# Optimization experiments

Measured on AMD Instinct MI355X. Metric: run time of the kernel, lower is better.

## Reference

```python
import jax, jax.numpy as jnp
import numpy as np

B, T, C, H = 2, 4096, 512, 8
D = C // H          # head_size = 64
FF = 4 * C          # 2048
EPS = 1e-5


def _layernorm(x, g, b):
    mu = jnp.mean(x, axis=-1, keepdims=True)
    var = jnp.mean(jnp.square(x - mu), axis=-1, keepdims=True)
    return (x - mu) * jax.lax.rsqrt(var + EPS) * g + b


def setup_inputs() -> dict:
    key = jax.random.key(0)
    ks = jax.random.split(key, 10)
    s = 0.02
    return {
        "x":  jax.random.normal(ks[0], (B, T, C), dtype=jnp.float32),
        # per-head K/Q/V linears (bias=False) packed as [C, C] = concat over heads
        "Wq": jax.random.normal(ks[1], (C, C), dtype=jnp.float32) * s,
        "Wk": jax.random.normal(ks[2], (C, C), dtype=jnp.float32) * s,
        "Wv": jax.random.normal(ks[3], (C, C), dtype=jnp.float32) * s,
        "Wo": jax.random.normal(ks[4], (C, C), dtype=jnp.float32) * s,
        "bo": jnp.zeros((C,), dtype=jnp.float32),
        "W1": jax.random.normal(ks[5], (C, FF), dtype=jnp.float32) * s,
        "b1": jnp.zeros((FF,), dtype=jnp.float32),
        "W2": jax.random.normal(ks[6], (FF, C), dtype=jnp.float32) * s,
        "b2": jnp.zeros((C,), dtype=jnp.float32),
        "g1": jnp.ones((C,), dtype=jnp.float32),
        "be1": jnp.zeros((C,), dtype=jnp.float32),
        "g2": jnp.ones((C,), dtype=jnp.float32),
        "be2": jnp.zeros((C,), dtype=jnp.float32),
    }


def reference(x, Wq, Wk, Wv, Wo, bo, W1, b1, W2, b2, g1, be1, g2, be2):
    # --- self-attention on ln1(x), residual add ---
    h = _layernorm(x, g1, be1)                              # [B,T,C]
    q = (h @ Wq).reshape(B, T, H, D)
    k = (h @ Wk).reshape(B, T, H, D)
    v = (h @ Wv).reshape(B, T, H, D)
    # NOTE: original scales by C**-0.5 (n_embd), NOT head_size**-0.5
    scores = jnp.einsum("bthd,bshd->bhts", q, k) * (C ** -0.5)  # [B,H,T,T]
    causal = jnp.tril(jnp.ones((T, T), dtype=bool))
    scores = jnp.where(causal, scores, -jnp.inf)
    wei = jax.nn.softmax(scores, axis=-1)                   # dropout = identity (eval)
    attn = jnp.einsum("bhts,bshd->bthd", wei, v).reshape(B, T, C)
    x = x + (attn @ Wo + bo)                                # proj dropout = identity
    # --- feed-forward on ln2(x), residual add ---
    h2 = _layernorm(x, g2, be2)
    ff = jax.nn.relu(h2 @ W1 + b1) @ W2 + b2                # dropout = identity
    return x + ff
```

## Files before the change

kernel.cpp:

```cpp
#include <hip/hip_runtime.h>

typedef __attribute__((ext_vector_type(8))) __bf16 bf16x8;
typedef __attribute__((ext_vector_type(4))) float f32x4;
typedef __attribute__((ext_vector_type(4))) unsigned int u32x4;
typedef __attribute__((ext_vector_type(4))) unsigned short u16x4;
typedef __attribute__((ext_vector_type(8))) unsigned short u16x8;
typedef unsigned short u16;

static __device__ __forceinline__ u16 f2b(float f) {
    unsigned u = __builtin_bit_cast(unsigned, f);
    u = (u + 0x7FFFu + ((u >> 16) & 1u)) >> 16;
    return (u16)u;
}
static __device__ __forceinline__ float b2f(u16 u) {
    return __builtin_bit_cast(float, ((unsigned)u) << 16);
}

static __device__ __forceinline__ void gload16(const u16* g, u16* l) {
    __builtin_amdgcn_global_load_lds(
        (const __attribute__((address_space(1))) unsigned int*)g,
        (__attribute__((address_space(3))) unsigned int*)l, 16, 0, 0);
}

__global__ __launch_bounds__(256) void prep_w(
    const float* __restrict__ Wq, const float* __restrict__ Wk,
    const float* __restrict__ Wv, const float* __restrict__ Wo,
    const float* __restrict__ W1, const float* __restrict__ W2,
    u16* __restrict__ WqkvT, u16* __restrict__ WoT,
    u16* __restrict__ W1T, u16* __restrict__ W2T)
{
    const int z = blockIdx.z;
    const float* src; u16* dst; int K, N;
    if (z == 0)      { src = Wq; dst = WqkvT;             K = 512;  N = 512;  }
    else if (z == 1) { src = Wk; dst = WqkvT + 512*512;   K = 512;  N = 512;  }
    else if (z == 2) { src = Wv; dst = WqkvT + 1024*512;  K = 512;  N = 512;  }
    else if (z == 3) { src = Wo; dst = WoT;               K = 512;  N = 512;  }
    else if (z == 4) { src = W1; dst = W1T;               K = 512;  N = 2048; }
    else             { src = W2; dst = W2T;               K = 2048; N = 512;  }
    const int nt = blockIdx.x * 32, kt = blockIdx.y * 32;
    if (nt >= N || kt >= K) return;
    __shared__ float tile[32][33];
    const int tx = threadIdx.x & 31, ty = threadIdx.x >> 5;
    #pragma unroll
    for (int i = 0; i < 4; ++i)
        tile[ty + i*8][tx] = src[(size_t)(kt + ty + i*8) * N + nt + tx];
    __syncthreads();
    #pragma unroll
    for (int i = 0; i < 4; ++i)
        dst[(size_t)(nt + ty + i*8) * K + kt + tx] = f2b(tile[tx][ty + i*8]);
}

__global__ __launch_bounds__(256) void ln_rows(
    const float* __restrict__ x, const float* __restrict__ g,
    const float* __restrict__ b, u16* __restrict__ out)
{
    const int row = blockIdx.x * 4 + (threadIdx.x >> 6);
    const int lane = threadIdx.x & 63;
    const float* xr = x + (size_t)row * 512;
    f32x4 v0 = *(const f32x4*)(xr + lane * 4);
    f32x4 v1 = *(const f32x4*)(xr + 256 + lane * 4);
    float s = v0[0]+v0[1]+v0[2]+v0[3]+v1[0]+v1[1]+v1[2]+v1[3];
    #pragma unroll
    for (int o = 1; o < 64; o <<= 1) s += __shfl_xor(s, o);
    const float mu = s * (1.0f / 512.0f);
    float s2 = 0.f;
    #pragma unroll
    for (int i = 0; i < 4; ++i) { float d0 = v0[i]-mu, d1 = v1[i]-mu; s2 += d0*d0 + d1*d1; }
    #pragma unroll
    for (int o = 1; o < 64; o <<= 1) s2 += __shfl_xor(s2, o);
    const float inv = rsqrtf(s2 * (1.0f/512.0f) + 1e-5f);
    f32x4 g0 = *(const f32x4*)(g + lane*4), g1 = *(const f32x4*)(g + 256 + lane*4);
    f32x4 b0 = *(const f32x4*)(b + lane*4), b1 = *(const f32x4*)(b + 256 + lane*4);
    u16x4 p0, p1;
    #pragma unroll
    for (int i = 0; i < 4; ++i) {
        p0[i] = f2b((v0[i]-mu)*inv*g0[i] + b0[i]);
        p1[i] = f2b((v1[i]-mu)*inv*g1[i] + b1[i]);
    }
    u16* orow = out + (size_t)row * 512;
    *(u16x4*)(orow + lane*4)       = p0;
    *(u16x4*)(orow + 256 + lane*4) = p1;
}

template<int FLAGS>
__global__ __launch_bounds__(256) void gemm_bt(
    const u16* __restrict__ A, const u16* __restrict__ BT,
    const int N, const int K,
    const float* __restrict__ bias, const float* __restrict__ res,
    void* __restrict__ outv)
{
    __shared__ __attribute__((aligned(16))) u16 As[128*32];
    __shared__ __attribute__((aligned(16))) u16 Bs[128*32];
    const int tid = threadIdx.x, lane = tid & 63, w = tid >> 6;
    const int wr = w >> 1, wc = w & 1;
    const int m0 = blockIdx.y << 7, n0 = blockIdx.x << 7;
    const int g = lane >> 4, c = lane & 15;
    const f32x4 fz = {0.f, 0.f, 0.f, 0.f};

    f32x4 acc[4][4];
    #pragma unroll
    for (int m = 0; m < 4; ++m)
      #pragma unroll
      for (int n = 0; n < 4; ++n) acc[m][n] = fz;

    const int srow = tid >> 2;
    const int scs = (((tid & 3) ^ (srow & 3)) * 8);
    const u16* Ag = A  + (size_t)(m0 + srow)*K + scs;
    const u16* Bg = BT + (size_t)(n0 + srow)*K + scs;
    const size_t rstep = (size_t)64 * K;
    u16* AsW = As + w*512;
    u16* BsW = Bs + w*512;

    const int nkt = K >> 5;
    for (int kt = 0; kt < nkt; ++kt) {
        const int k0 = kt << 5;
        gload16(Ag + k0,         AsW);
        gload16(Ag + rstep + k0, AsW + 2048);
        gload16(Bg + k0,         BsW);
        gload16(Bg + rstep + k0, BsW + 2048);
        __syncthreads();
        bf16x8 af[4], bfr[4];
        #pragma unroll
        for (int m = 0; m < 4; ++m) {
            const int row = wr*64 + m*16 + c;
            af[m] = *(const bf16x8*)(As + row*32 + (((g*16) ^ ((row&3)<<4)) >> 1));
        }
        #pragma unroll
        for (int n = 0; n < 4; ++n) {
            const int row = wc*64 + n*16 + c;
            bfr[n] = *(const bf16x8*)(Bs + row*32 + (((g*16) ^ ((row&3)<<4)) >> 1));
        }
        #pragma unroll
        for (int m = 0; m < 4; ++m)
          #pragma unroll
          for (int n = 0; n < 4; ++n)
            acc[m][n] = __builtin_amdgcn_mfma_f32_16x16x32_bf16(af[m], bfr[n], acc[m][n], 0, 0, 0);
        __syncthreads();
    }

    #pragma unroll
    for (int m = 0; m < 4; ++m) {
        const int row = m0 + wr*64 + m*16 + 4*g;
        #pragma unroll
        for (int n = 0; n < 4; ++n) {
            const int col = n0 + wc*64 + n*16 + c;
            const float bv = (FLAGS & 1) ? bias[col] : 0.0f;
            #pragma unroll
            for (int r = 0; r < 4; ++r) {
                float v = acc[m][n][r] + bv;
                if (FLAGS & 2) v += res[(size_t)(row + r)*N + col];
                if (FLAGS & 4) v = fmaxf(v, 0.0f);
                if (FLAGS & 8) ((float*)outv)[(size_t)(row + r)*N + col] = v;
                else           ((u16*)outv)[(size_t)(row + r)*N + col] = f2b(v);
            }
        }
    }
}

__global__ __launch_bounds__(256) void transpose_v(
    const u16* __restrict__ qkv, u16* __restrict__ vT)
{
    const int b = blockIdx.z;
    const int t0 = blockIdx.x * 32, c0 = blockIdx.y * 32;
    __shared__ u16 tile[32][33];
    const int tx = threadIdx.x & 31, ty = threadIdx.x >> 5;
    #pragma unroll
    for (int i = 0; i < 4; ++i)
        tile[ty + i*8][tx] =
            qkv[(size_t)(b*4096 + t0 + ty + i*8)*1536 + 1024 + c0 + tx];
    __syncthreads();
    #pragma unroll
    for (int i = 0; i < 4; ++i)
        vT[(size_t)(b*512 + c0 + ty + i*8)*4096 + t0 + tx] = tile[tx][ty + i*8];
}

__global__ __launch_bounds__(256) void attn_fwd(
    const u16* __restrict__ qkv, const u16* __restrict__ vT, u16* __restrict__ part)
{
    const int bh = blockIdx.y, b = bh >> 3, h = bh & 7;
    const int i = blockIdx.x;
    int q, cch;
    if (i < 16)      { q = i;                       cch = 0; }
    else if (i < 48) { int j = i-16; q = 16 + (j>>1); cch = j & 1; }
    else if (i < 96) { int j = i-48; int d = j/3; q = 32 + d; cch = j - 3*d; }
    else             { int j = i-96; q = 48 + (j>>2); cch = j & 3; }
    const int t0 = cch*16;
    const int t1e = t0 + 16, t1 = (t1e < q+1) ? t1e : q+1;

    const int tid = threadIdx.x, lane = tid & 63, w = tid >> 6;
    const int g = lane >> 4, c16 = lane & 15;
    __shared__ __attribute__((aligned(16))) u16 Ks[2][4096];
    __shared__ __attribute__((aligned(16))) u16 Vs[2][4096];
    __shared__ __attribute__((aligned(16))) u16 Ps[4][16*72];

    const u16* qp  = qkv + (size_t)b*4096*1536 + h*64;
    const u16* kp  = qp + 512;
    const u16* vtp = vT + (size_t)bh*64*4096;

    const int srow = tid >> 3;
    const int scs  = (((tid & 7) ^ (srow & 7)) * 8);
    const u16* kg0 = kp + (size_t)srow*1536 + scs;
    const u16* kg1 = kg0 + (size_t)32*1536;
    const u16* vg0 = vtp + (size_t)srow*4096 + scs;
    const u16* vg1 = vg0 + (size_t)32*4096;
    u16* KsW0 = &Ks[0][0] + w*512;  u16* VsW0 = &Vs[0][0] + w*512;
    u16* KsW1 = &Ks[1][0] + w*512;  u16* VsW1 = &Vs[1][0] + w*512;

    const int q0w = q*64 + w*16;
    const bf16x8 qf0 = *(const bf16x8*)(qp + (size_t)(q0w + c16)*1536 + g*8);
    const bf16x8 qf1 = *(const bf16x8*)(qp + (size_t)(q0w + c16)*1536 + 32 + g*8);

    const f32x4 fz = {0.f, 0.f, 0.f, 0.f};
    f32x4 oacc[4] = {fz, fz, fz, fz};
    float lsum[4] = {0.f, 0.f, 0.f, 0.f};
    const float scale = 0.04419417382415922f;
    u16* Pw = &Ps[w][0];

    const int rA = c16;
    const int jx = (g ^ (rA & 7)) * 8, jy = ((4+g) ^ (rA & 7)) * 8;

    {
        const size_t kvo = (size_t)(t0 << 6);
        gload16(kg0 + kvo*1536, KsW0); gload16(kg1 + kvo*1536, KsW0 + 2048);
        gload16(vg0 + kvo,      VsW0); gload16(vg1 + kvo,      VsW0 + 2048);
    }
    __syncthreads();

    int buf = 0;
    for (int t = t0; t < t1; ++t) {
        if (t + 1 < t1) {
            const size_t kvo = (size_t)((t+1) << 6);
            u16* kd = buf ? KsW0 : KsW1;
            u16* vd = buf ? VsW0 : VsW1;
            gload16(kg0 + kvo*1536, kd); gload16(kg1 + kvo*1536, kd + 2048);
            gload16(vg0 + kvo,      vd); gload16(vg1 + kvo,      vd + 2048);
        }
        const u16* Kb = &Ks[buf][0];
        const u16* Vb = &Vs[buf][0];
        const int kv0 = t << 6;

        f32x4 s[4];
        #pragma unroll
        for (int sub = 0; sub < 4; ++sub) {
            const int ro = (sub*16 + c16) * 64;
            bf16x8 kb0 = *(const bf16x8*)(Kb + ro + jx);
            bf16x8 kb1 = *(const bf16x8*)(Kb + ro + jy);
            f32x4 sv = fz;
            sv = __builtin_amdgcn_mfma_f32_16x16x32_bf16(qf0, kb0, sv, 0, 0, 0);
            sv = __builtin_amdgcn_mfma_f32_16x16x32_bf16(qf1, kb1, sv, 0, 0, 0);
            s[sub] = sv;
        }
        const bool fullt = (kv0 + 63 <= q0w);
        if (fullt) {
            #pragma unroll
            for (int sub = 0; sub < 4; ++sub)
              #pragma unroll
              for (int r = 0; r < 4; ++r) {
                  float p = __expf(s[sub][r] * scale);
                  lsum[r] += p;
                  Pw[(4*g + r)*72 + sub*16 + c16] = f2b(p);
              }
        } else {
            #pragma unroll
            for (int sub = 0; sub < 4; ++sub)
              #pragma unroll
              for (int r = 0; r < 4; ++r) {
                  const int qi = q0w + 4*g + r;
                  const int kv = kv0 + sub*16 + c16;
                  float p = (kv <= qi) ? __expf(s[sub][r] * scale) : 0.0f;
                  lsum[r] += p;
                  Pw[(4*g + r)*72 + sub*16 + c16] = f2b(p);
              }
        }
        const bf16x8 pa0 = *(const bf16x8*)(Pw + c16*72 + g*8);
        const bf16x8 pa1 = *(const bf16x8*)(Pw + c16*72 + 32 + g*8);
        #pragma unroll
        for (int dt = 0; dt < 4; ++dt) {
            const int ro = (dt*16 + c16) * 64;
            bf16x8 vb0 = *(const bf16x8*)(Vb + ro + jx);
            bf16x8 vb1 = *(const bf16x8*)(Vb + ro + jy);
            oacc[dt] = __builtin_amdgcn_mfma_f32_16x16x32_bf16(pa0, vb0, oacc[dt], 0, 0, 0);
            oacc[dt] = __builtin_amdgcn_mfma_f32_16x16x32_bf16(pa1, vb1, oacc[dt], 0, 0, 0);
        }
        __syncthreads();
        buf ^= 1;
    }

    #pragma unroll
    for (int r = 0; r < 4; ++r) {
        float v = lsum[r];
        v += __shfl_xor(v, 1); v += __shfl_xor(v, 2);
        v += __shfl_xor(v, 4); v += __shfl_xor(v, 8);
        lsum[r] = v;
    }

    u16* onum = part + (size_t)(bh*160 + i) * 4224;
    float* lout = (float*)(onum + 4096);
    const int qloc = w*16 + 4*g;
    #pragma unroll
    for (int r = 0; r < 4; ++r) {
        #pragma unroll
        for (int dt = 0; dt < 4; ++dt)
            onum[(qloc + r)*64 + dt*16 + c16] = f2b(oacc[dt][r]);
        if (c16 == 0) lout[qloc + r] = lsum[r];
    }
}

__global__ __launch_bounds__(256) void attn_merge(
    const u16* __restrict__ part, u16* __restrict__ att)
{
    const int q = blockIdx.x, bh = blockIdx.y, b = bh >> 3, h = bh & 7;
    int start, n;
    if (q < 16)      { start = q;               n = 1; }
    else if (q < 32) { start = 16 + 2*(q-16);   n = 2; }
    else if (q < 48) { start = 48 + 3*(q-32);   n = 3; }
    else             { start = 96 + 4*(q-48);   n = 4; }
    const int t = threadIdx.x;
    const int row = t >> 2, c0 = (t & 3) * 16;
    float acc[16];
    #pragma unroll
    for (int j = 0; j < 16; ++j) acc[j] = 0.f;
    float lt = 0.f;
    const u16* p0 = part + (size_t)(bh*160 + start) * 4224;
    for (int ci = 0; ci < n; ++ci) {
        const u16* pc = p0 + (size_t)ci * 4224;
        lt += ((const float*)(pc + 4096))[row];
        u16x8 a = *(const u16x8*)(pc + row*64 + c0);
        u16x8 bq = *(const u16x8*)(pc + row*64 + c0 + 8);
        #pragma unroll
        for (int j = 0; j < 8; ++j) { acc[j] += b2f(a[j]); acc[8+j] += b2f(bq[j]); }
    }
    const float inv = 1.0f / lt;
    u16x8 o1, o2;
    #pragma unroll
    for (int j = 0; j < 8; ++j) { o1[j] = f2b(acc[j]*inv); o2[j] = f2b(acc[8+j]*inv); }
    u16* dst = att + (size_t)(b*4096 + q*64 + row)*512 + h*64 + c0;
    *(u16x8*)dst = o1;
    *(u16x8*)(dst + 8) = o2;
}

extern "C" void kernel_launch(void* const* d_in, const int* in_sizes, int n_in,
                              void* d_out, int out_size, void* d_ws, size_t ws_size,
                              hipStream_t stream)
{
    (void)in_sizes; (void)n_in; (void)out_size; (void)ws_size;
    const float* x   = (const float*)d_in[0];
    const float* Wq  = (const float*)d_in[1];
    const float* Wk  = (const float*)d_in[2];
    const float* Wv  = (const float*)d_in[3];
    const float* Wo  = (const float*)d_in[4];
    const float* bo  = (const float*)d_in[5];
    const float* W1  = (const float*)d_in[6];
    const float* b1  = (const float*)d_in[7];
    const float* W2  = (const float*)d_in[8];
    const float* b2  = (const float*)d_in[9];
    const float* g1  = (const float*)d_in[10];
    const float* be1 = (const float*)d_in[11];
    const float* g2  = (const float*)d_in[12];
    const float* be2 = (const float*)d_in[13];

    char* ws = (char*)d_ws;
    u16*   WqkvT = (u16*)(ws + 0);
    u16*   WoT   = (u16*)(ws + 1572864);
    u16*   W1T   = (u16*)(ws + 2097152);
    u16*   W2T   = (u16*)(ws + 4194304);
    u16*   H     = (u16*)(ws + 6291456);
    u16*   PART  = (u16*)(ws + 6291456);
    float* X2    = (float*)(ws + 14680064);
    u16*   QKV   = (u16*)(ws + 31457280);
    u16*   VT    = (u16*)(ws + 56623104);
    u16*   ATT   = (u16*)(ws + 65011712);
    u16*   F1    = (u16*)(ws + 31457280);

    prep_w<<<dim3(64, 64, 6), 256, 0, stream>>>(Wq, Wk, Wv, Wo, W1, W2,
                                                WqkvT, WoT, W1T, W2T);
    ln_rows<<<2048, 256, 0, stream>>>(x, g1, be1, H);
    gemm_bt<0><<<dim3(12, 64), 256, 0, stream>>>(H, WqkvT, 1536, 512,
                                                 nullptr, nullptr, QKV);
    transpose_v<<<dim3(128, 16, 2), 256, 0, stream>>>(QKV, VT);
    attn_fwd<<<dim3(160, 16), 256, 0, stream>>>(QKV, VT, PART);
    attn_merge<<<dim3(64, 16), 256, 0, stream>>>(PART, ATT);
    gemm_bt<11><<<dim3(4, 64), 256, 0, stream>>>(ATT, WoT, 512, 512,
                                                 bo, x, X2);
    ln_rows<<<2048, 256, 0, stream>>>(X2, g2, be2, H);
    gemm_bt<5><<<dim3(16, 64), 256, 0, stream>>>(H, W1T, 2048, 512,
                                                 b1, nullptr, F1);
    gemm_bt<11><<<dim3(4, 64), 256, 0, stream>>>(F1, W2T, 512, 2048,
                                                 b2, X2, (float*)d_out);
}
```

Measured before the change: 234.0 us.

## Restructure attention to split KV across waves, keep P in registers, prescale Q

After: 232.2 us. Within noise of the previous version (-0.8%).

```diff
diff --git a/kernel.cpp b/kernel.cpp
--- a/kernel.cpp
+++ b/kernel.cpp
@@ -1,10 +1,12 @@
 #include <hip/hip_runtime.h>
 
 typedef __attribute__((ext_vector_type(8))) __bf16 bf16x8;
+typedef __attribute__((ext_vector_type(4))) __bf16 bf16x4;
 typedef __attribute__((ext_vector_type(4))) float f32x4;
 typedef __attribute__((ext_vector_type(4))) unsigned int u32x4;
 typedef __attribute__((ext_vector_type(4))) unsigned short u16x4;
 typedef __attribute__((ext_vector_type(8))) unsigned short u16x8;
+typedef __attribute__((ext_vector_type(4))) short s16x4;
 typedef unsigned short u16;
 
 static __device__ __forceinline__ u16 f2b(float f) {
@@ -14,6 +16,21 @@
 }
 static __device__ __forceinline__ float b2f(u16 u) {
     return __builtin_bit_cast(float, ((unsigned)u) << 16);
+}
+static __device__ __forceinline__ float fexp2(float x) {
+#if __has_builtin(__builtin_amdgcn_exp2f)
+    return __builtin_amdgcn_exp2f(x);
+#else
+    return exp2f(x);
+#endif
+}
+static __device__ __forceinline__ f32x4 mfma16(bf16x4 a, bf16x4 b, f32x4 c) {
+#if __has_builtin(__builtin_amdgcn_mfma_f32_16x16x16_bf16)
+    return __builtin_amdgcn_mfma_f32_16x16x16_bf16(a, b, c, 0, 0, 0);
+#else
+    return __builtin_amdgcn_mfma_f32_16x16x16bf16_1k(
+        __builtin_bit_cast(s16x4, a), __builtin_bit_cast(s16x4, b), c, 0, 0, 0);
+#endif
 }
 
 static __device__ __forceinline__ void gload16(const u16* g, u16* l) {
@@ -145,9 +162,11 @@
         for (int n = 0; n < 4; ++n) {
             const int col = n0 + wc*64 + n*16 + c;
             const float bv = (FLAGS & 1) ? bias[col] : 0.0f;
+            const float qs = (FLAGS & 16) ? ((col < 512) ? 0.0637587246f : 1.0f) : 1.0f;
             #pragma unroll
             for (int r = 0; r < 4; ++r) {
                 float v = acc[m][n][r] + bv;
+                if (FLAGS & 16) v *= qs;
                 if (FLAGS & 2) v += res[(size_t)(row + r)*N + col];
                 if (FLAGS & 4) v = fmaxf(v, 0.0f);
                 if (FLAGS & 8) ((float*)outv)[(size_t)(row + r)*N + col] = v;
@@ -179,19 +198,19 @@
 {
     const int bh = blockIdx.y, b = bh >> 3, h = bh & 7;
     const int i = blockIdx.x;
-    int q, cch;
-    if (i < 16)      { q = i;                       cch = 0; }
-    else if (i < 48) { int j = i-16; q = 16 + (j>>1); cch = j & 1; }
-    else if (i < 96) { int j = i-48; int d = j/3; q = 32 + d; cch = j - 3*d; }
-    else             { int j = i-96; q = 48 + (j>>2); cch = j & 3; }
+    int qt, cch;
+    if (i < 16)      { qt = i;                        cch = 0; }
+    else if (i < 48) { int j = i-16; qt = 16 + (j>>1); cch = j & 1; }
+    else if (i < 96) { int j = i-48; int d = j/3; qt = 32 + d; cch = j - 3*d; }
+    else             { int j = i-96; qt = 48 + (j>>2); cch = j & 3; }
     const int t0 = cch*16;
-    const int t1e = t0 + 16, t1 = (t1e < q+1) ? t1e : q+1;
+    const int t1e = t0 + 16, t1 = (t1e < qt+1) ? t1e : qt+1;
 
     const int tid = threadIdx.x, lane = tid & 63, w = tid >> 6;
     const int g = lane >> 4, c16 = lane & 15;
-    __shared__ __attribute__((aligned(16))) u16 Ks[2][4096];
-    __shared__ __attribute__((aligned(16))) u16 Vs[2][4096];
-    __shared__ __attribute__((aligned(16))) u16 Ps[4][16*72];
+    __shared__ __attribute__((aligned(16))) u16 smem[16896];
+    u16* Ks0 = smem;          u16* Ks1 = smem + 4096;
+    u16* Vs0 = smem + 8192;   u16* Vs1 = smem + 12288;
 
     const u16* qp  = qkv + (size_t)b*4096*1536 + h*64;
     const u16* kp  = qp + 512;
@@ -203,21 +222,30 @@
     const u16* kg1 = kg0 + (size_t)32*1536;
     const u16* vg0 = vtp + (size_t)srow*4096 + scs;
     const u16* vg1 = vg0 + (size_t)32*4096;
-    u16* KsW0 = &Ks[0][0] + w*512;  u16* VsW0 = &Vs[0][0] + w*512;
-    u16* KsW1 = &Ks[1][0] + w*512;  u16* VsW1 = &Vs[1][0] + w*512;
-
-    const int q0w = q*64 + w*16;
-    const bf16x8 qf0 = *(const bf16x8*)(qp + (size_t)(q0w + c16)*1536 + g*8);
-    const bf16x8 qf1 = *(const bf16x8*)(qp + (size_t)(q0w + c16)*1536 + 32 + g*8);
-
-    const f32x4 fz = {0.f, 0.f, 0.f, 0.f};
-    f32x4 oacc[4] = {fz, fz, fz, fz};
+    u16* KsW0 = Ks0 + w*512;  u16* VsW0 = Vs0 + w*512;
+    u16* KsW1 = Ks1 + w*512;  u16* VsW1 = Vs1 + w*512;
+
+    const int Q0 = qt*64;
+    bf16x8 qB[4][2];
+    #pragma unroll
+    for (int sub = 0; sub < 4; ++sub) {
+        const u16* qr = qp + (size_t)(Q0 + sub*16 + c16)*1536 + g*8;
+        qB[sub][0] = *(const bf16x8*)(qr);
+        qB[sub][1] = *(const bf16x8*)(qr + 32);
+    }
+
+    const f32x4 fz = {0.f,0.f,0.f,0.f};
+    f32x4 oacc[4][4];
+    #pragma unroll
+    for (int dt = 0; dt < 4; ++dt)
+      #pragma unroll
+      for (int sub = 0; sub < 4; ++sub) oacc[dt][sub] = fz;
     float lsum[4] = {0.f, 0.f, 0.f, 0.f};
-    const float scale = 0.04419417382415922f;
-    u16* Pw = &Ps[w][0];
-
-    const int rA = c16;
-    const int jx = (g ^ (rA & 7)) * 8, jy = ((4+g) ^ (rA & 7)) * 8;
+
+    const int kRow  = 16*w + c16;
+    const int kOff0 = kRow*64 + ((g    ) ^ (c16 & 7))*8;
+    const int kOff1 = kRow*64 + ((4 + g) ^ (c16 & 7))*8;
+    const int vChk  = ((2*w + (g >> 1)) ^ (c16 & 7))*8 + (g & 1)*4;
 
     {
         const size_t kvo = (size_t)(t0 << 6);
@@ -235,74 +263,120 @@
             gload16(kg0 + kvo*1536, kd); gload16(kg1 + kvo*1536, kd + 2048);
             gload16(vg0 + kvo,      vd); gload16(vg1 + kvo,      vd + 2048);
         }
-        const u16* Kb = &Ks[buf][0];
-        const u16* Vb = &Vs[buf][0];
-        const int kv0 = t << 6;
-
+        const u16* Kb = buf ? Ks1 : Ks0;
+        const u16* Vb = buf ? Vs1 : Vs0;
+
+        const bf16x8 kA0 = *(const bf16x8*)(Kb + kOff0);
+        const bf16x8 kA1 = *(const bf16x8*)(Kb + kOff1);
         f32x4 s[4];
         #pragma unroll
         for (int sub = 0; sub < 4; ++sub) {
-            const int ro = (sub*16 + c16) * 64;
-            bf16x8 kb0 = *(const bf16x8*)(Kb + ro + jx);
-            bf16x8 kb1 = *(const bf16x8*)(Kb + ro + jy);
-            f32x4 sv = fz;
-            sv = __builtin_amdgcn_mfma_f32_16x16x32_bf16(qf0, kb0, sv, 0, 0, 0);
-            sv = __builtin_amdgcn_mfma_f32_16x16x32_bf16(qf1, kb1, sv, 0, 0, 0);
-            s[sub] = sv;
-        }
-        const bool fullt = (kv0 + 63 <= q0w);
-        if (fullt) {
-            #pragma unroll
-            for (int sub = 0; sub < 4; ++sub)
-              #pragma unroll
-              for (int r = 0; r < 4; ++r) {
-                  float p = __expf(s[sub][r] * scale);
-                  lsum[r] += p;
-                  Pw[(4*g + r)*72 + sub*16 + c16] = f2b(p);
-              }
+            f32x4 sv = __builtin_amdgcn_mfma_f32_16x16x32_bf16(kA0, qB[sub][0], fz, 0, 0, 0);
+            s[sub]   = __builtin_amdgcn_mfma_f32_16x16x32_bf16(kA1, qB[sub][1], sv, 0, 0, 0);
+        }
+        bf16x4 va[4];
+        #pragma unroll
+        for (int dt = 0; dt < 4; ++dt)
+            va[dt] = *(const bf16x4*)(Vb + (dt*16 + c16)*64 + vChk);
+        bf16x4 pt[4];
+        if (t < qt) {
+            #pragma unroll
+            for (int sub = 0; sub < 4; ++sub) {
+                float p0 = fexp2(s[sub][0]), p1 = fexp2(s[sub][1]);
+                float p2 = fexp2(s[sub][2]), p3 = fexp2(s[sub][3]);
+                lsum[sub] += (p0 + p1) + (p2 + p3);
+                bf16x4 pv;
+                pv[0] = (__bf16)p0; pv[1] = (__bf16)p1;
+                pv[2] = (__bf16)p2; pv[3] = (__bf16)p3;
+                pt[sub] = pv;
+            }
         } else {
-            #pragma unroll
-            for (int sub = 0; sub < 4; ++sub)
-              #pragma unroll
-              for (int r = 0; r < 4; ++r) {
-                  const int qi = q0w + 4*g + r;
-                  const int kv = kv0 + sub*16 + c16;
-                  float p = (kv <= qi) ? __expf(s[sub][r] * scale) : 0.0f;
-                  lsum[r] += p;
-                  Pw[(4*g + r)*72 + sub*16 + c16] = f2b(p);
-              }
-        }
-        const bf16x8 pa0 = *(const bf16x8*)(Pw + c16*72 + g*8);
-        const bf16x8 pa1 = *(const bf16x8*)(Pw + c16*72 + 32 + g*8);
-        #pragma unroll
-        for (int dt = 0; dt < 4; ++dt) {
-            const int ro = (dt*16 + c16) * 64;
-            bf16x8 vb0 = *(const bf16x8*)(Vb + ro + jx);
-            bf16x8 vb1 = *(const bf16x8*)(Vb + ro + jy);
-            oacc[dt] = __builtin_amdgcn_mfma_f32_16x16x32_bf16(pa0, vb0, oacc[dt], 0, 0, 0);
-            oacc[dt] = __builtin_amdgcn_mfma_f32_16x16x32_bf16(pa1, vb1, oacc[dt], 0, 0, 0);
-        }
+            const int kvbase = t*64 + 16*w + 4*g;
+            #pragma unroll
+            for (int sub = 0; sub < 4; ++sub) {
+                const int qi = Q0 + sub*16 + c16;
+                bf16x4 pv; float a = 0.f;
+                #pragma unroll
+                for (int r = 0; r < 4; ++r) {
+                    float p = (kvbase + r <= qi) ? fexp2(s[sub][r]) : 0.0f;
+                    a += p; pv[r] = (__bf16)p;
+                }
+                lsum[sub] += a; pt[sub] = pv;
+            }
+        }
+        #pragma unroll
+        for (int dt = 0; dt < 4; ++dt)
+          #pragma unroll
+          for (int sub = 0; sub < 4; ++sub)
+            oacc[dt][sub] = mfma16(va[dt], pt[sub], oacc[dt][sub]);
         __syncthreads();
         buf ^= 1;
     }
 
     #pragma unroll
-    for (int r = 0; r < 4; ++r) {
-        float v = lsum[r];
-        v += __shfl_xor(v, 1); v += __shfl_xor(v, 2);
-        v += __shfl_xor(v, 4); v += __shfl_xor(v, 8);
-        lsum[r] = v;
-    }
-
-    u16* onum = part + (size_t)(bh*160 + i) * 4224;
-    float* lout = (float*)(onum + 4096);
-    const int qloc = w*16 + 4*g;
-    #pragma unroll
-    for (int r = 0; r < 4; ++r) {
-        #pragma unroll
-        for (int dt = 0; dt < 4; ++dt)
-            onum[(qloc + r)*64 + dt*16 + c16] = f2b(oacc[dt][r]);
-        if (c16 == 0) lout[qloc + r] = lsum[r];
+    for (int sub = 0; sub < 4; ++sub) {
+        float v = lsum[sub];
+        v += __shfl_xor(v, 16);
+        v += __shfl_xor(v, 32);
+        lsum[sub] = v;
+    }
+
+    float* red  = (float*)smem;
+    float* lbuf = (float*)smem + 8192;
+    if (g == 0) {
+        #pragma unroll
+        for (int sub = 0; sub < 4; ++sub) lbuf[w*64 + sub*16 + c16] = lsum[sub];
+    }
+    if (w >= 2) {
+        float* img = red + (w & 1)*4096;
+        #pragma unroll
+        for (int sub = 0; sub < 4; ++sub) {
+            const int ro = (sub*16 + c16)*64;
+            #pragma unroll
+            for (int dt = 0; dt < 4; ++dt)
+                *(f32x4*)(img + ro + ((dt*4 + g) ^ c16)*4) = oacc[dt][sub];
+        }
+    }
+    __syncthreads();
+    if (w < 2) {
+        float* img = red + w*4096;
+        #pragma unroll
+        for (int sub = 0; sub < 4; ++sub) {
+            const int ro = (sub*16 + c16)*64;
+            #pragma unroll
+            for (int dt = 0; dt < 4; ++dt)
+                oacc[dt][sub] += *(const f32x4*)(img + ro + ((dt*4 + g) ^ c16)*4);
+        }
+    }
+    __syncthreads();
+    if (w == 1) {
+        #pragma unroll
+        for (int sub = 0; sub < 4; ++sub) {
+            const int ro = (sub*16 + c16)*64;
+            #pragma unroll
+            for (int dt = 0; dt < 4; ++dt)
+                *(f32x4*)(red + ro + ((dt*4 + g) ^ c16)*4) = oacc[dt][sub];
+        }
+    }
+    __syncthreads();
+    if (w == 0) {
+        u16* onum = part + (size_t)(bh*160 + i) * 4224;
+        float* lout = (float*)(onum + 4096);
+        #pragma unroll
+        for (int sub = 0; sub < 4; ++sub) {
+            const int qrow = sub*16 + c16;
+            const int ro = qrow*64;
+            #pragma unroll
+            for (int dt = 0; dt < 4; ++dt) {
+                f32x4 o = oacc[dt][sub] + *(const f32x4*)(red + ro + ((dt*4 + g) ^ c16)*4);
+                bf16x4 ov;
+                ov[0] = (__bf16)o[0]; ov[1] = (__bf16)o[1];
+                ov[2] = (__bf16)o[2]; ov[3] = (__bf16)o[3];
+                *(u16x4*)(onum + qrow*64 + dt*16 + 4*g) = __builtin_bit_cast(u16x4, ov);
+            }
+            if (g == 0)
+                lout[qrow] = lbuf[qrow] + lbuf[64 + qrow] + lbuf[128 + qrow] + lbuf[192 + qrow];
+        }
     }
 }
 
@@ -375,8 +449,8 @@
     prep_w<<<dim3(64, 64, 6), 256, 0, stream>>>(Wq, Wk, Wv, Wo, W1, W2,
                                                 WqkvT, WoT, W1T, W2T);
     ln_rows<<<2048, 256, 0, stream>>>(x, g1, be1, H);
-    gemm_bt<0><<<dim3(12, 64), 256, 0, stream>>>(H, WqkvT, 1536, 512,
-                                                 nullptr, nullptr, QKV);
+    gemm_bt<16><<<dim3(12, 64), 256, 0, stream>>>(H, WqkvT, 1536, 512,
+                                                  nullptr, nullptr, QKV);
     transpose_v<<<dim3(128, 16, 2), 256, 0, stream>>>(QKV, VT);
     attn_fwd<<<dim3(160, 16), 256, 0, stream>>>(QKV, VT, PART);
     attn_merge<<<dim3(64, 16), 256, 0, stream>>>(PART, ATT);
```
